# Optimization experiments

Hardware: AMD Instinct MI355X
Metric: run time of the kernel (lower is better)

## Reference

```python
import jax, jax.numpy as jnp
import numpy as np

# --- constants from the module (KANLayer passes degree=3; BSplineActivation defaults) ---
K = 5          # num_control_points
DEG = 3        # degree
G = 3          # grid points (set_grid_points(3) in __init__)
LO, HI = -1.0, 1.0  # grid_range


def basis_table():
    """Precompute the shared [G, K] normalized Gaussian basis table (same for all edges)."""
    knots = np.linspace(LO - DEG * 0.1, HI + DEG * 0.1, K + DEG + 1)
    grid = np.linspace(LO, HI, G)
    bv = np.zeros((G, K), dtype=np.float32)
    for i in range(K):
        center = (knots[i + DEG // 2] + knots[i + DEG // 2 + 1]) / 2.0
        width = (knots[i + DEG + 1] - knots[i]) / 2.0
        bv[:, i] = np.exp(-(((grid - center) / width) ** 2))
    bv = bv / (bv.sum(axis=1, keepdims=True) + 1e-6)
    return jnp.asarray(bv)


def kan_layer(x, cp, bw, sw, imp, bv):
    """Fused KANLayer: x [B,I]; cp [I,J,K]; bw/sw/imp [I,J]; bv [G,K] -> [B,J]."""
    xc = jnp.clip(x, LO, HI)
    gi = (xc - LO) / (HI - LO) * (G - 1)                     # [B,I] in [0, G-1]
    lo = jnp.clip(jnp.floor(gi).astype(jnp.int32), 0, G - 1)
    hi = jnp.clip(jnp.ceil(gi).astype(jnp.int32), 0, G - 1)
    frac = (gi - lo.astype(gi.dtype))[..., None]             # [B,I,1]
    basis = bv[lo] * (1.0 - frac) + bv[hi] * frac            # [B,I,K] gather + lerp
    base = x * jax.nn.sigmoid(x)                             # SiLU base function, [B,I]
    # out[b,j] = sum_i imp[i,j] * (bw[i,j]*base[b,i] + sw[i,j]*basis[b,i,:]@cp[i,j,:])
    out = jnp.einsum('bi,ij->bj', base, imp * bw)
    out = out + jnp.einsum('bik,ijk->bj', basis, imp[:, :, None] * sw[:, :, None] * cp)
    return out


def setup_inputs() -> dict:
    key = jax.random.key(0)
    ks = jax.random.split(key, 9)
    B, D0, D1, D2 = 131072, 64, 128, 64
    return {
        'x': jax.random.normal(ks[0], (B, D0), dtype=jnp.float32),
        'cp0': jax.random.normal(ks[1], (D0, D1, K), dtype=jnp.float32) * 0.1,
        'bw0': jax.random.normal(ks[2], (D0, D1), dtype=jnp.float32),
        'sw0': jax.random.normal(ks[3], (D0, D1), dtype=jnp.float32),
        'imp0': jnp.ones((D0, D1), dtype=jnp.float32),
        'cp1': jax.random.normal(ks[4], (D1, D2, K), dtype=jnp.float32) * 0.1,
        'bw1': jax.random.normal(ks[5], (D1, D2), dtype=jnp.float32),
        'sw1': jax.random.normal(ks[6], (D1, D2), dtype=jnp.float32),
        'imp1': jnp.ones((D1, D2), dtype=jnp.float32),
    }


def reference(x, cp0, bw0, sw0, imp0, cp1, bw1, sw1, imp1):
    bv = basis_table()
    h = kan_layer(x, cp0, bw0, sw0, imp0, bv)
    return kan_layer(h, cp1, bw1, sw1, imp1, bv)
```

## Files before the change

### kernel.cpp

```cpp
#include <hip/hip_runtime.h>
#include <math.h>

typedef __attribute__((ext_vector_type(8))) _Float16 f16x8;
typedef __attribute__((ext_vector_type(2))) _Float16 f16x2;
typedef __attribute__((ext_vector_type(4))) float f32x4;


#define TPB 256
#define BM  128
#define HSTRIDE 272
#define LDS_TOT (128 * HSTRIDE)

__global__ __launch_bounds__(TPB, 2) void kan_mfma_kernel(
    const float* __restrict__ x, const _Float16* __restrict__ W0t,
    const _Float16* __restrict__ W1t, const float* __restrict__ bias0,
    const float* __restrict__ bias1, float* __restrict__ out)
{
    __shared__ char smem[LDS_TOT];
    const int tid  = threadIdx.x;
    const int lane = tid & 63;
    const int wid  = tid >> 6;
    const int gq   = lane >> 4;
    const int lm   = lane & 15;
    const int wavebase = wid * 32;
    const long rowbase = (long)blockIdx.x * BM;

#if __has_builtin(__builtin_amdgcn_cvt_pkrtz)
    auto pk2 = [](float a, float b) -> f16x2 {
        return (f16x2)__builtin_amdgcn_cvt_pkrtz(a, b);
    };
#else
    auto pk2 = [](float a, float b) -> f16x2 {
        return f16x2{(_Float16)a, (_Float16)b};
    };
#endif
#if __has_builtin(__builtin_amdgcn_rcpf)
    auto frcp = [](float a) -> float { return __builtin_amdgcn_rcpf(a); };
#else
    auto frcp = [](float a) -> float { return 1.0f / a; };
#endif

    auto buildFeats4 = [&](const float* v, f16x8* dst) {
        union U { f16x8 v8; f16x2 h2[4]; } u0, u1, u2, u3;
        #pragma unroll
        for (int q = 0; q < 4; ++q) {
            float va = v[2 * q], vb = v[2 * q + 1];
            float ba = va * frcp(1.0f + __expf(-va));
            float bb = vb * frcp(1.0f + __expf(-vb));
            float ga = fminf(fmaxf(va, -1.f), 1.f) + 1.f;
            float gb = fminf(fmaxf(vb, -1.f), 1.f) + 1.f;
            float s1a = (ga >= 1.f) ? 1.f : 0.f;
            float s1b = (gb >= 1.f) ? 1.f : 0.f;
            float sga = (ga >= 1.f) ? ga : 0.f;
            float sgb = (gb >= 1.f) ? gb : 0.f;
            u0.h2[q] = pk2(ba, bb);
            u1.h2[q] = pk2(ga, gb);
            u2.h2[q] = pk2(s1a, s1b);
            u3.h2[q] = pk2(sga, sgb);
        }
        dst[0] = u0.v8; dst[1] = u1.v8; dst[2] = u2.v8; dst[3] = u3.v8;
    };

    float b0v[8], b1v[4];
    #pragma unroll
    for (int nf = 0; nf < 8; ++nf) b0v[nf] = bias0[nf * 16 + lm];
    #pragma unroll
    for (int nf = 0; nf < 4; ++nf) b1v[nf] = bias1[nf * 16 + lm];

    float v0[2][8], v1[2][8];
    #pragma unroll
    for (int mi = 0; mi < 2; ++mi) {
        const float* xp = x + (rowbase + wavebase + mi * 16 + lm) * 64 + gq * 8;
        float4 a0 = *(const float4*)(xp);
        float4 a1 = *(const float4*)(xp + 4);
        float4 a2 = *(const float4*)(xp + 32);
        float4 a3 = *(const float4*)(xp + 36);
        v0[mi][0]=a0.x; v0[mi][1]=a0.y; v0[mi][2]=a0.z; v0[mi][3]=a0.w;
        v0[mi][4]=a1.x; v0[mi][5]=a1.y; v0[mi][6]=a1.z; v0[mi][7]=a1.w;
        v1[mi][0]=a2.x; v1[mi][1]=a2.y; v1[mi][2]=a2.z; v1[mi][3]=a2.w;
        v1[mi][4]=a3.x; v1[mi][5]=a3.y; v1[mi][6]=a3.z; v1[mi][7]=a3.w;
    }

    f32x4 acc[2][8] = {};
    {
        const char* w0 = (const char*)W0t + gq * 2048 + lm * 16;
        f16x8 b0[8], b1[8];
        #pragma unroll
        for (int nf = 0; nf < 8; ++nf) b0[nf] = *(const f16x8*)(w0 + nf * 256);

        f16x8 fr[2][4];
        buildFeats4(v0[0], fr[0]);
        buildFeats4(v0[1], fr[1]);

#define L0_STEP(S, C, CUR, NXT) do {                                          \
        if ((S) < 7) {                                                        \
            _Pragma("unroll")                                                 \
            for (int nf = 0; nf < 8; ++nf)                                    \
                NXT[nf] = *(const f16x8*)(w0 + ((S) + 1) * 8192 + nf * 256);  \
        }                                                                     \
        _Pragma("unroll")                                                     \
        for (int mi = 0; mi < 2; ++mi) {                                      \
            f16x8 a = fr[mi][C];                                              \
            _Pragma("unroll")                                                 \
            for (int nf = 0; nf < 8; ++nf)                                    \
                acc[mi][nf] = __builtin_amdgcn_mfma_f32_16x16x32_f16(         \
                    a, CUR[nf], acc[mi][nf], 0, 0, 0);                        \
        }                                                                     \
    } while (0)

        L0_STEP(0, 0, b0, b1); L0_STEP(1, 1, b1, b0);
        L0_STEP(2, 2, b0, b1); L0_STEP(3, 3, b1, b0);
        buildFeats4(v1[0], fr[0]);
        buildFeats4(v1[1], fr[1]);
        L0_STEP(4, 0, b0, b1); L0_STEP(5, 1, b1, b0);
        L0_STEP(6, 2, b0, b1); L0_STEP(7, 3, b1, b0);
#undef L0_STEP
    }

    #pragma unroll
    for (int mi = 0; mi < 2; ++mi)
        #pragma unroll
        for (int nf = 0; nf < 8; ++nf)
            #pragma unroll
            for (int rg = 0; rg < 4; ++rg)
                *(_Float16*)(smem + (wavebase + mi * 16 + gq * 4 + rg) * HSTRIDE
                             + (nf * 16 + lm) * 2) = (_Float16)(acc[mi][nf][rg] + b0v[nf]);
    __syncthreads();

    f32x4 accO[2][4] = {};
    #pragma unroll
    for (int half = 0; half < 2; ++half) {
        float hv0[2][8], hv1[2][8];
        #pragma unroll
        for (int mi = 0; mi < 2; ++mi) {
            const char* hrow = smem + (wavebase + mi * 16 + lm) * HSTRIDE;
            f16x8 ha = *(const f16x8*)(hrow + (half * 64 + gq * 8) * 2);
            f16x8 hb = *(const f16x8*)(hrow + (half * 64 + 32 + gq * 8) * 2);
            #pragma unroll
            for (int e = 0; e < 8; ++e) { hv0[mi][e] = (float)ha[e]; hv1[mi][e] = (float)hb[e]; }
        }

        const char* w1 = (const char*)W1t + half * 32768 + gq * 1024 + lm * 16;
        f16x8 c0[4], c1[4];
        #pragma unroll
        for (int nf = 0; nf < 4; ++nf) c0[nf] = *(const f16x8*)(w1 + nf * 256);

        f16x8 fr[2][4];
        buildFeats4(hv0[0], fr[0]);
        buildFeats4(hv0[1], fr[1]);

#define L1_STEP(S, C, CUR, NXT) do {                                          \
        if ((S) < 7) {                                                        \
            _Pragma("unroll")                                                 \
            for (int nf = 0; nf < 4; ++nf)                                    \
                NXT[nf] = *(const f16x8*)(w1 + ((S) + 1) * 4096 + nf * 256);  \
        }                                                                     \
        _Pragma("unroll")                                                     \
        for (int mi = 0; mi < 2; ++mi) {                                      \
            f16x8 a = fr[mi][C];                                              \
            _Pragma("unroll")                                                 \
            for (int nf = 0; nf < 4; ++nf)                                    \
                accO[mi][nf] = __builtin_amdgcn_mfma_f32_16x16x32_f16(        \
                    a, CUR[nf], accO[mi][nf], 0, 0, 0);                       \
        }                                                                     \
    } while (0)

        L1_STEP(0, 0, c0, c1); L1_STEP(1, 1, c1, c0);
        L1_STEP(2, 2, c0, c1); L1_STEP(3, 3, c1, c0);
        buildFeats4(hv1[0], fr[0]);
        buildFeats4(hv1[1], fr[1]);
        L1_STEP(4, 0, c0, c1); L1_STEP(5, 1, c1, c0);
        L1_STEP(6, 2, c0, c1); L1_STEP(7, 3, c1, c0);
#undef L1_STEP
    }

    float* og = out + (rowbase + wavebase) * 64;
    #pragma unroll
    for (int mi = 0; mi < 2; ++mi)
        #pragma unroll
        for (int nf = 0; nf < 4; ++nf)
            #pragma unroll
            for (int rg = 0; rg < 4; ++rg)
                og[(mi * 16 + gq * 4 + rg) * 64 + nf * 16 + lm] = accO[mi][nf][rg] + b1v[nf];
}

__global__ __launch_bounds__(256) void kan_combine_w(
    const float* __restrict__ cp0, const float* __restrict__ bw0,
    const float* __restrict__ sw0, const float* __restrict__ imp0,
    const float* __restrict__ cp1, const float* __restrict__ bw1,
    const float* __restrict__ sw1, const float* __restrict__ imp1,
    _Float16* __restrict__ W0t, _Float16* __restrict__ W1t,
    float* __restrict__ bias0, float* __restrict__ bias1)
{
    float bvv[3][5];
    #pragma unroll
    for (int g = 0; g < 3; ++g) {
        float gv = (float)g - 1.0f;
        float e[5]; float s = 0.f;
        #pragma unroll
        for (int i = 0; i < 5; ++i) {
            float cc = -0.8125f + 0.325f * (float)i;
            float d  = (gv - cc) * (1.0f / 0.65f);
            e[i] = __expf(-d * d); s += e[i];
        }
        float inv = 1.0f / (s + 1e-6f);
        #pragma unroll
        for (int i = 0; i < 5; ++i) bvv[g][i] = e[i] * inv;
    }

    auto wval = [&](const float* cp, float bw, float sw, float imp, int q) -> float {
        if (q == 0) return imp * bw;
        float P0 = 0.f, Q0 = 0.f, P1 = 0.f, Q1 = 0.f;
        #pragma unroll
        for (int c = 0; c < 5; ++c) {
            P0 += cp[c] * bvv[0][c];
            Q0 += cp[c] * (bvv[1][c] - bvv[0][c]);
            P1 += cp[c] * (2.f * bvv[1][c] - bvv[2][c]);
            Q1 += cp[c] * (bvv[2][c] - bvv[1][c]);
        }
        float r = (q == 1) ? Q0 : (q == 2) ? (P1 - P0) : (Q1 - Q0);
        return imp * sw * r;
    };
    auto p0val = [&](const float* cp) -> float {
        float P0 = 0.f;
        #pragma unroll
        for (int c = 0; c < 5; ++c) P0 += cp[c] * bvv[0][c];
        return P0;
    };

    const int bx = blockIdx.x;
    const int t  = threadIdx.x;

    if (bx < 256) {
        int f = bx * 256 + t;
        if (f < 32768) {
            int e = f & 7, n = (f >> 3) & 127, g = (f >> 10) & 3, s = f >> 12;
            int ih = s >> 2, q = s & 3;
            int i = ih * 32 + g * 8 + e;
            int edge = i * 128 + n;
            W0t[f] = (_Float16)wval(cp0 + edge * 5, bw0[edge], sw0[edge], imp0[edge], q);
        } else {
            int f2 = f - 32768;
            int e = f2 & 7, n = (f2 >> 3) & 63, g = (f2 >> 9) & 3;
            int tq = f2 >> 11;
            int half = tq >> 3, s = tq & 7;
            int ih = s >> 2, q = s & 3;
            int i2 = half * 64 + ih * 32 + g * 8 + e;
            int edge = i2 * 64 + n;
            W1t[f2] = (_Float16)wval(cp1 + edge * 5, bw1[edge], sw1[edge], imp1[edge], q);
        }
    } else if (bx == 256) {
        __shared__ float part[256];
        int j = t >> 1, h = t & 1;
        float s = 0.f;
        #pragma unroll 4
        for (int i = h * 32; i < h * 32 + 32; ++i) {
            int edge = i * 128 + j;
            s += imp0[edge] * sw0[edge] * p0val(cp0 + edge * 5);
        }
        part[t] = s;
        __syncthreads();
        if (t < 128) bias0[t] = part[2 * t] + part[2 * t + 1];
    } else {
        __shared__ float part[256];
        int j = t >> 2, qtr = t & 3;
        float s = 0.f;
        #pragma unroll 4
        for (int i2 = qtr * 32; i2 < qtr * 32 + 32; ++i2) {
            int edge = i2 * 64 + j;
            s += imp1[edge] * sw1[edge] * p0val(cp1 + edge * 5);
        }
        part[t] = s;
        __syncthreads();
        if (t < 64) bias1[t] = part[4 * t] + part[4 * t + 1] + part[4 * t + 2] + part[4 * t + 3];
    }
}

#define NTHR 256
#define JT 32
#define WS8 8

#define STAGE_L0(JBASE) do {                                                  \
    _Pragma("unroll")                                                         \
    for (int p = 0; p < 8; ++p) {                                             \
        int idx = tid + p * NTHR;                                             \
        int i  = idx >> 5;                                                    \
        int jj = idx & 31;                                                    \
        int e  = i * 128 + (JBASE) + jj;                                      \
        float im = imp0[e];                                                   \
        float wb = bw0[e] * im;                                               \
        float ws = sw0[e] * im;                                               \
        const float* cp = cp0 + e * 5;                                        \
        float* wp = wbuf + idx * WS8;                                         \
        wp[0] = wb;                                                           \
        wp[1] = ws * cp[0]; wp[2] = ws * cp[1]; wp[3] = ws * cp[2];           \
        wp[4] = ws * cp[3]; wp[5] = ws * cp[4];                               \
    }                                                                         \
} while (0)

#define STAGE_L1(IBASE, JBASE) do {                                           \
    _Pragma("unroll")                                                         \
    for (int p = 0; p < 8; ++p) {                                             \
        int idx = tid + p * NTHR;                                             \
        int ii = idx >> 5;                                                    \
        int jj = idx & 31;                                                    \
        int e  = ((IBASE) + ii) * 64 + (JBASE) + jj;                          \
        float im = imp1[e];                                                   \
        float wb = bw1[e] * im;                                               \
        float ws = sw1[e] * im;                                               \
        const float* cp = cp1 + e * 5;                                        \
        float* wp = wbuf + idx * WS8;                                         \
        wp[0] = wb;                                                           \
        wp[1] = ws * cp[0]; wp[2] = ws * cp[1]; wp[3] = ws * cp[2];           \
        wp[4] = ws * cp[3]; wp[5] = ws * cp[4];                               \
    }                                                                         \
} while (0)

#define COMPUTE_TILE(ACC) do {                                                \
    _Pragma("unroll 2")                                                       \
    for (int i = 0; i < 64; ++i) {                                            \
        float v  = vbuf[i][tid];                                              \
        float sg = 1.0f / (1.0f + __expf(-v));                                \
        float base = v * sg;                                                  \
        float xc = fminf(fmaxf(v, -1.0f), 1.0f);                              \
        float gi = xc + 1.0f;                                                 \
        int lo = (int)gi; lo = (lo > 2) ? 2 : lo;                             \
        float fr = gi - (float)lo;                                            \
        int hi = (fr > 0.0f) ? (lo + 1) : lo;                                 \
        float b0 = bvt[lo][0]; b0 += (bvt[hi][0] - b0) * fr;                  \
        float b1 = bvt[lo][1]; b1 += (bvt[hi][1] - b1) * fr;                  \
        float b2 = bvt[lo][2]; b2 += (bvt[hi][2] - b2) * fr;                  \
        float b3 = bvt[lo][3]; b3 += (bvt[hi][3] - b3) * fr;                  \
        float b4 = bvt[lo][4]; b4 += (bvt[hi][4] - b4) * fr;                  \
        const float* wr = wbuf + i * (JT * WS8);                              \
        _Pragma("unroll")                                                     \
        for (int jj = 0; jj < JT; ++jj) {                                     \
            const float* wp = wr + jj * WS8;                                  \
            float a = ACC[jj];                                                \
            a = fmaf(wp[0], base, a);                                         \
            a = fmaf(wp[1], b0, a);                                           \
            a = fmaf(wp[2], b1, a);                                           \
            a = fmaf(wp[3], b2, a);                                           \
            a = fmaf(wp[4], b3, a);                                           \
            a = fmaf(wp[5], b4, a);                                           \
            ACC[jj] = a;                                                      \
        }                                                                     \
    }                                                                         \
} while (0)

__global__ __launch_bounds__(NTHR) void kan_fused_kernel(
    const float* __restrict__ x,
    const float* __restrict__ cp0, const float* __restrict__ bw0,
    const float* __restrict__ sw0, const float* __restrict__ imp0,
    const float* __restrict__ cp1, const float* __restrict__ bw1,
    const float* __restrict__ sw1, const float* __restrict__ imp1,
    float* __restrict__ out)
{
    __shared__ float vbuf[64][NTHR + 1];
    __shared__ float wbuf[64 * JT * WS8];
    __shared__ float bvt[3][8];

    const int tid = threadIdx.x;

    if (tid < 3) {
        float gv = -1.0f + (float)tid;
        float e[5];
        float s = 0.0f;
        #pragma unroll
        for (int i = 0; i < 5; ++i) {
            float c = -0.8125f + 0.325f * (float)i;
            float d = (gv - c) * (1.0f / 0.65f);
            e[i] = expf(-d * d);
            s += e[i];
        }
        float inv = 1.0f / (s + 1e-6f);
        #pragma unroll
        for (int i = 0; i < 5; ++i) bvt[tid][i] = e[i] * inv;
    }

    {
        const float4* xg = (const float4*)(x + (size_t)blockIdx.x * (NTHR * 64));
        #pragma unroll
        for (int it = 0; it < 16; ++it) {
            int e4 = tid + it * NTHR;
            float4 v = xg[e4];
            int r  = e4 >> 4;
            int ib = (e4 & 15) << 2;
            vbuf[ib + 0][r] = v.x;
            vbuf[ib + 1][r] = v.y;
            vbuf[ib + 2][r] = v.z;
            vbuf[ib + 3][r] = v.w;
        }
    }
    __syncthreads();

    float h0[32] = {}, h1[32] = {}, h2[32] = {}, h3[32] = {};
    STAGE_L0(0);   __syncthreads(); COMPUTE_TILE(h0); __syncthreads();
    STAGE_L0(32);  __syncthreads(); COMPUTE_TILE(h1); __syncthreads();
    STAGE_L0(64);  __syncthreads(); COMPUTE_TILE(h2); __syncthreads();
    STAGE_L0(96);  __syncthreads(); COMPUTE_TILE(h3); __syncthreads();

    #pragma unroll
    for (int i = 0; i < 32; ++i) vbuf[i][tid] = h0[i];
    #pragma unroll
    for (int i = 0; i < 32; ++i) vbuf[32 + i][tid] = h1[i];

    float o0[32] = {}, o1[32] = {};
    STAGE_L1(0, 0);   __syncthreads(); COMPUTE_TILE(o0); __syncthreads();
    STAGE_L1(0, 32);  __syncthreads(); COMPUTE_TILE(o1); __syncthreads();

    #pragma unroll
    for (int i = 0; i < 32; ++i) vbuf[i][tid] = h2[i];
    #pragma unroll
    for (int i = 0; i < 32; ++i) vbuf[32 + i][tid] = h3[i];

    STAGE_L1(64, 0);  __syncthreads(); COMPUTE_TILE(o0); __syncthreads();
    STAGE_L1(64, 32); __syncthreads(); COMPUTE_TILE(o1);

    float4* og = (float4*)(out + (size_t)blockIdx.x * (NTHR * 64) + (size_t)tid * 64);
    #pragma unroll
    for (int q = 0; q < 8; ++q)
        og[q] = make_float4(o0[4 * q + 0], o0[4 * q + 1], o0[4 * q + 2], o0[4 * q + 3]);
    #pragma unroll
    for (int q = 0; q < 8; ++q)
        og[8 + q] = make_float4(o1[4 * q + 0], o1[4 * q + 1], o1[4 * q + 2], o1[4 * q + 3]);
}

extern "C" void kernel_launch(void* const* d_in, const int* in_sizes, int n_in,
                              void* d_out, int out_size, void* d_ws, size_t ws_size,
                              hipStream_t stream) {
    const float* x    = (const float*)d_in[0];
    const float* cp0  = (const float*)d_in[1];
    const float* bw0  = (const float*)d_in[2];
    const float* sw0  = (const float*)d_in[3];
    const float* imp0 = (const float*)d_in[4];
    const float* cp1  = (const float*)d_in[5];
    const float* bw1  = (const float*)d_in[6];
    const float* sw1  = (const float*)d_in[7];
    const float* imp1 = (const float*)d_in[8];
    float* out = (float*)d_out;

    const int B = in_sizes[0] / 64;
    const size_t need = 65536 * sizeof(_Float16) + 192 * sizeof(float);

    if (ws_size >= need && (B % BM) == 0) {
        _Float16* W0t = (_Float16*)d_ws;
        _Float16* W1t = W0t + 32768;
        float* bias0 = (float*)(W1t + 32768);
        float* bias1 = bias0 + 128;
        kan_combine_w<<<258, 256, 0, stream>>>(cp0, bw0, sw0, imp0,
                                               cp1, bw1, sw1, imp1,
                                               W0t, W1t, bias0, bias1);
        kan_mfma_kernel<<<B / BM, TPB, 0, stream>>>(x, W0t, W1t, bias0, bias1, out);
    } else {
        kan_fused_kernel<<<B / NTHR, NTHR, 0, stream>>>(
            x, cp0, bw0, sw0, imp0, cp1, bw1, sw1, imp1, out);
    }
}
```

Baseline: 42.11 us.

## Add per-step workgroup barriers in MFMA loops and widen weight-combine blocks

Puts an s_barrier after every MFMA step in both layer loops so the waves of a workgroup stay in lockstep, which may help share cached weight loads between waves. It also relaunches the weight-combine kernel with 1024-thread blocks and 66 blocks instead of 258, and splits the bias reductions across more threads so each one has a shorter serial loop. The barriers add stalls to the hot loop, and the bigger combine blocks may lower occupancy.

```diff
diff --git a/kernel.cpp b/kernel.cpp
--- a/kernel.cpp
+++ b/kernel.cpp
@@ -106,6 +106,7 @@
                 acc[mi][nf] = __builtin_amdgcn_mfma_f32_16x16x32_f16(         \
                     a, CUR[nf], acc[mi][nf], 0, 0, 0);                        \
         }                                                                     \
+        __builtin_amdgcn_s_barrier();    \
     } while (0)
 
         L0_STEP(0, 0, b0, b1); L0_STEP(1, 1, b1, b0);
@@ -163,6 +164,7 @@
                 accO[mi][nf] = __builtin_amdgcn_mfma_f32_16x16x32_f16(        \
                     a, CUR[nf], accO[mi][nf], 0, 0, 0);                       \
         }                                                                     \
+        __builtin_amdgcn_s_barrier();                                         \
     } while (0)
 
         L1_STEP(0, 0, c0, c1); L1_STEP(1, 1, c1, c0);
@@ -184,7 +186,7 @@
                 og[(mi * 16 + gq * 4 + rg) * 64 + nf * 16 + lm] = accO[mi][nf][rg] + b1v[nf];
 }
 
-__global__ __launch_bounds__(256) void kan_combine_w(
+__global__ __launch_bounds__(1024) void kan_combine_w(
     const float* __restrict__ cp0, const float* __restrict__ bw0,
     const float* __restrict__ sw0, const float* __restrict__ imp0,
     const float* __restrict__ cp1, const float* __restrict__ bw1,
@@ -231,8 +233,8 @@
     const int bx = blockIdx.x;
     const int t  = threadIdx.x;
 
-    if (bx < 256) {
-        int f = bx * 256 + t;
+    if (bx < 64) {
+        int f = bx * 1024 + t;
         if (f < 32768) {
             int e = f & 7, n = (f >> 3) & 127, g = (f >> 10) & 3, s = f >> 12;
             int ih = s >> 2, q = s & 3;
@@ -249,30 +251,42 @@
             int edge = i2 * 64 + n;
             W1t[f2] = (_Float16)wval(cp1 + edge * 5, bw1[edge], sw1[edge], imp1[edge], q);
         }
-    } else if (bx == 256) {
-        __shared__ float part[256];
-        int j = t >> 1, h = t & 1;
+    } else if (bx == 64) {
+        __shared__ float part[1024];
+        int j = t >> 3, split = t & 7;
         float s = 0.f;
-        #pragma unroll 4
-        for (int i = h * 32; i < h * 32 + 32; ++i) {
+        #pragma unroll
+        for (int k = 0; k < 8; ++k) {
+            int i = split * 8 + k;
             int edge = i * 128 + j;
             s += imp0[edge] * sw0[edge] * p0val(cp0 + edge * 5);
         }
         part[t] = s;
         __syncthreads();
-        if (t < 128) bias0[t] = part[2 * t] + part[2 * t + 1];
+        if (t < 128) {
+            float acc = 0.f;
+            #pragma unroll
+            for (int k = 0; k < 8; ++k) acc += part[t * 8 + k];
+            bias0[t] = acc;
+        }
     } else {
-        __shared__ float part[256];
-        int j = t >> 2, qtr = t & 3;
+        __shared__ float part[1024];
+        int j = t >> 4, split = t & 15;
         float s = 0.f;
-        #pragma unroll 4
-        for (int i2 = qtr * 32; i2 < qtr * 32 + 32; ++i2) {
+        #pragma unroll
+        for (int k = 0; k < 8; ++k) {
+            int i2 = split * 8 + k;
             int edge = i2 * 64 + j;
             s += imp1[edge] * sw1[edge] * p0val(cp1 + edge * 5);
         }
         part[t] = s;
         __syncthreads();
-        if (t < 64) bias1[t] = part[4 * t] + part[4 * t + 1] + part[4 * t + 2] + part[4 * t + 3];
+        if (t < 64) {
+            float acc = 0.f;
+            #pragma unroll
+            for (int k = 0; k < 16; ++k) acc += part[t * 16 + k];
+            bias1[t] = acc;
+        }
     }
 }
 
@@ -448,7 +462,7 @@
         _Float16* W1t = W0t + 32768;
         float* bias0 = (float*)(W1t + 32768);
         float* bias1 = bias0 + 128;
-        kan_combine_w<<<258, 256, 0, stream>>>(cp0, bw0, sw0, imp0,
+        kan_combine_w<<<66, 1024, 0, stream>>>(cp0, bw0, sw0, imp0,
                                                cp1, bw1, sw1, imp1,
                                                W0t, W1t, bias0, bias1);
         kan_mfma_kernel<<<B / BM, TPB, 0, stream>>>(x, W0t, W1t, bias0, bias1, out);
```

Result: slower. 49.65 us (+17.9%).

## Stage MFMA weight tiles through double-buffered LDS and parallelize bias reduction

Applied to the files above, without the earlier changes.

Previously each wave loaded its B-operand weight fragments straight from global memory, so all four waves re-read the same weights. The new code has the whole block cooperatively copy each weight chunk into a double-buffered LDS region, with prefetch into registers and a __syncthreads per step. This cuts redundant global/L2 traffic but adds 8+16 block barriers and grows LDS from about 35KB to about 51KB. The bias-reduction blocks in the combine kernel are also spread across 16+16 blocks instead of 2 to shorten that serial tail.

```diff
diff --git a/kernel.cpp b/kernel.cpp
--- a/kernel.cpp
+++ b/kernel.cpp
@@ -9,7 +9,8 @@
 #define TPB 256
 #define BM  128
 #define HSTRIDE 272
-#define LDS_TOT (128 * HSTRIDE)
+#define W_OFF   34816
+#define LDS_TOT (34816 + 16384)
 
 __global__ __launch_bounds__(TPB, 2) void kan_mfma_kernel(
     const float* __restrict__ x, const _Float16* __restrict__ W0t,
@@ -83,95 +84,120 @@
 
     f32x4 acc[2][8] = {};
     {
-        const char* w0 = (const char*)W0t + gq * 2048 + lm * 16;
-        f16x8 b0[8], b1[8];
-        #pragma unroll
-        for (int nf = 0; nf < 8; ++nf) b0[nf] = *(const f16x8*)(w0 + nf * 256);
-
+        const char* w0 = (const char*)W0t;
+        const int lb0 = (gq * 128 + lm) * 16;
+
+        {
+            float4 pa = *(const float4*)(w0 + tid * 32);
+            float4 pb = *(const float4*)(w0 + tid * 32 + 16);
+            *(float4*)(smem + W_OFF + tid * 32)      = pa;
+            *(float4*)(smem + W_OFF + tid * 32 + 16) = pb;
+        }
         f16x8 fr[2][4];
         buildFeats4(v0[0], fr[0]);
         buildFeats4(v0[1], fr[1]);
-
-#define L0_STEP(S, C, CUR, NXT) do {                                          \
+        __syncthreads();
+
+        float4 wr0, wr1;
+#define L0_STEP(S, C) do {                                                    \
         if ((S) < 7) {                                                        \
-            _Pragma("unroll")                                                 \
-            for (int nf = 0; nf < 8; ++nf)                                    \
-                NXT[nf] = *(const f16x8*)(w0 + ((S) + 1) * 8192 + nf * 256);  \
+            wr0 = *(const float4*)(w0 + ((S) + 1) * 8192 + tid * 32);         \
+            wr1 = *(const float4*)(w0 + ((S) + 1) * 8192 + tid * 32 + 16);    \
         }                                                                     \
+        const char* wb = smem + W_OFF + ((S) & 1) * 8192;                     \
+        f16x8 bt[8];                                                          \
+        _Pragma("unroll")                                                     \
+        for (int nf = 0; nf < 8; ++nf)                                        \
+            bt[nf] = *(const f16x8*)(wb + lb0 + nf * 256);                    \
         _Pragma("unroll")                                                     \
         for (int mi = 0; mi < 2; ++mi) {                                      \
             f16x8 a = fr[mi][C];                                              \
             _Pragma("unroll")                                                 \
             for (int nf = 0; nf < 8; ++nf)                                    \
                 acc[mi][nf] = __builtin_amdgcn_mfma_f32_16x16x32_f16(         \
-                    a, CUR[nf], acc[mi][nf], 0, 0, 0);                        \
+                    a, bt[nf], acc[mi][nf], 0, 0, 0);                         \
         }                                                                     \
+        if ((S) < 7) {                                                        \
+            char* nb = smem + W_OFF + (((S) + 1) & 1) * 8192;                 \
+            *(float4*)(nb + tid * 32)      = wr0;                             \
+            *(float4*)(nb + tid * 32 + 16) = wr1;                             \
+        }                                                                     \
+        __syncthreads();                                                      \
     } while (0)
 
-        L0_STEP(0, 0, b0, b1); L0_STEP(1, 1, b1, b0);
-        L0_STEP(2, 2, b0, b1); L0_STEP(3, 3, b1, b0);
+        L0_STEP(0, 0); L0_STEP(1, 1); L0_STEP(2, 2); L0_STEP(3, 3);
         buildFeats4(v1[0], fr[0]);
         buildFeats4(v1[1], fr[1]);
-        L0_STEP(4, 0, b0, b1); L0_STEP(5, 1, b1, b0);
-        L0_STEP(6, 2, b0, b1); L0_STEP(7, 3, b1, b0);
+        L0_STEP(4, 0); L0_STEP(5, 1); L0_STEP(6, 2); L0_STEP(7, 3);
 #undef L0_STEP
     }
 
-    #pragma unroll
-    for (int mi = 0; mi < 2; ++mi)
-        #pragma unroll
-        for (int nf = 0; nf < 8; ++nf)
+    {
+        const char* w1 = (const char*)W1t;
+        float4 p0 = *(const float4*)(w1 + tid * 16);
+        #pragma unroll
+        for (int mi = 0; mi < 2; ++mi)
             #pragma unroll
-            for (int rg = 0; rg < 4; ++rg)
-                *(_Float16*)(smem + (wavebase + mi * 16 + gq * 4 + rg) * HSTRIDE
-                             + (nf * 16 + lm) * 2) = (_Float16)(acc[mi][nf][rg] + b0v[nf]);
-    __syncthreads();
+            for (int nf = 0; nf < 8; ++nf)
+                #pragma unroll
+                for (int rg = 0; rg < 4; ++rg)
+                    *(_Float16*)(smem + (wavebase + mi * 16 + gq * 4 + rg) * HSTRIDE
+                                 + (nf * 16 + lm) * 2) = (_Float16)(acc[mi][nf][rg] + b0v[nf]);
+        __syncthreads();
+        *(float4*)(smem + W_OFF + tid * 16) = p0;
+        __syncthreads();
+    }
 
     f32x4 accO[2][4] = {};
-    #pragma unroll
-    for (int half = 0; half < 2; ++half) {
-        float hv0[2][8], hv1[2][8];
-        #pragma unroll
-        for (int mi = 0; mi < 2; ++mi) {
-            const char* hrow = smem + (wavebase + mi * 16 + lm) * HSTRIDE;
-            f16x8 ha = *(const f16x8*)(hrow + (half * 64 + gq * 8) * 2);
-            f16x8 hb = *(const f16x8*)(hrow + (half * 64 + 32 + gq * 8) * 2);
-            #pragma unroll
-            for (int e = 0; e < 8; ++e) { hv0[mi][e] = (float)ha[e]; hv1[mi][e] = (float)hb[e]; }
-        }
-
-        const char* w1 = (const char*)W1t + half * 32768 + gq * 1024 + lm * 16;
-        f16x8 c0[4], c1[4];
-        #pragma unroll
-        for (int nf = 0; nf < 4; ++nf) c0[nf] = *(const f16x8*)(w1 + nf * 256);
-
+    {
+        const char* w1 = (const char*)W1t;
+        const int lb1 = (gq * 64 + lm) * 16;
         f16x8 fr[2][4];
-        buildFeats4(hv0[0], fr[0]);
-        buildFeats4(hv0[1], fr[1]);
-
-#define L1_STEP(S, C, CUR, NXT) do {                                          \
-        if ((S) < 7) {                                                        \
-            _Pragma("unroll")                                                 \
-            for (int nf = 0; nf < 4; ++nf)                                    \
-                NXT[nf] = *(const f16x8*)(w1 + ((S) + 1) * 4096 + nf * 256);  \
-        }                                                                     \
+        float4 wr0;
+
+#define L1_STEP(CI, C) do {                                                   \
+        if ((CI) < 15)                                                        \
+            wr0 = *(const float4*)(w1 + ((CI) + 1) * 4096 + tid * 16);        \
+        const char* wb = smem + W_OFF + ((CI) & 1) * 8192;                    \
+        f16x8 bt[4];                                                          \
+        _Pragma("unroll")                                                     \
+        for (int nf = 0; nf < 4; ++nf)                                        \
+            bt[nf] = *(const f16x8*)(wb + lb1 + nf * 256);                    \
         _Pragma("unroll")                                                     \
         for (int mi = 0; mi < 2; ++mi) {                                      \
             f16x8 a = fr[mi][C];                                              \
             _Pragma("unroll")                                                 \
             for (int nf = 0; nf < 4; ++nf)                                    \
                 accO[mi][nf] = __builtin_amdgcn_mfma_f32_16x16x32_f16(        \
-                    a, CUR[nf], accO[mi][nf], 0, 0, 0);                       \
+                    a, bt[nf], accO[mi][nf], 0, 0, 0);                        \
+        }                                                                     \
+        if ((CI) < 15)                                                        \
+            *(float4*)(smem + W_OFF + (((CI) + 1) & 1) * 8192 + tid * 16) = wr0; \
+        __syncthreads();                                                      \
+    } while (0)
+
+#define L1_FEATS(HALF, IH) do {                                               \
+        _Pragma("unroll")                                                     \
+        for (int mi = 0; mi < 2; ++mi) {                                      \
+            const char* hrow = smem + (wavebase + mi * 16 + lm) * HSTRIDE;    \
+            f16x8 hv = *(const f16x8*)(hrow + ((HALF) * 64 + (IH) * 32 + gq * 8) * 2); \
+            float v[8];                                                       \
+            _Pragma("unroll")                                                 \
+            for (int e = 0; e < 8; ++e) v[e] = (float)hv[e];                  \
+            buildFeats4(v, fr[mi]);                                           \
         }                                                                     \
     } while (0)
 
-        L1_STEP(0, 0, c0, c1); L1_STEP(1, 1, c1, c0);
-        L1_STEP(2, 2, c0, c1); L1_STEP(3, 3, c1, c0);
-        buildFeats4(hv1[0], fr[0]);
-        buildFeats4(hv1[1], fr[1]);
-        L1_STEP(4, 0, c0, c1); L1_STEP(5, 1, c1, c0);
-        L1_STEP(6, 2, c0, c1); L1_STEP(7, 3, c1, c0);
+        L1_FEATS(0, 0);
+        L1_STEP(0, 0);  L1_STEP(1, 1);  L1_STEP(2, 2);  L1_STEP(3, 3);
+        L1_FEATS(0, 1);
+        L1_STEP(4, 0);  L1_STEP(5, 1);  L1_STEP(6, 2);  L1_STEP(7, 3);
+        L1_FEATS(1, 0);
+        L1_STEP(8, 0);  L1_STEP(9, 1);  L1_STEP(10, 2); L1_STEP(11, 3);
+        L1_FEATS(1, 1);
+        L1_STEP(12, 0); L1_STEP(13, 1); L1_STEP(14, 2); L1_STEP(15, 3);
 #undef L1_STEP
+#undef L1_FEATS
     }
 
     float* og = out + (rowbase + wavebase) * 64;
@@ -249,30 +275,46 @@
             int edge = i2 * 64 + n;
             W1t[f2] = (_Float16)wval(cp1 + edge * 5, bw1[edge], sw1[edge], imp1[edge], q);
         }
-    } else if (bx == 256) {
+    } else if (bx < 272) {
         __shared__ float part[256];
-        int j = t >> 1, h = t & 1;
+        int bb = bx - 256;
+        int jj = t >> 5, split = t & 31;
+        int j = bb * 8 + jj;
         float s = 0.f;
-        #pragma unroll 4
-        for (int i = h * 32; i < h * 32 + 32; ++i) {
+        #pragma unroll
+        for (int k = 0; k < 2; ++k) {
+            int i = split * 2 + k;
             int edge = i * 128 + j;
             s += imp0[edge] * sw0[edge] * p0val(cp0 + edge * 5);
         }
         part[t] = s;
         __syncthreads();
-        if (t < 128) bias0[t] = part[2 * t] + part[2 * t + 1];
+        if (t < 8) {
+            float acc = 0.f;
+            #pragma unroll
+            for (int k = 0; k < 32; ++k) acc += part[t * 32 + k];
+            bias0[bb * 8 + t] = acc;
+        }
     } else {
         __shared__ float part[256];
-        int j = t >> 2, qtr = t & 3;
+        int bb = bx - 272;
+        int jj = t >> 6, split = t & 63;
+        int j = bb * 4 + jj;
         float s = 0.f;
-        #pragma unroll 4
-        for (int i2 = qtr * 32; i2 < qtr * 32 + 32; ++i2) {
+        #pragma unroll
+        for (int k = 0; k < 2; ++k) {
+            int i2 = split * 2 + k;
             int edge = i2 * 64 + j;
             s += imp1[edge] * sw1[edge] * p0val(cp1 + edge * 5);
         }
         part[t] = s;
         __syncthreads();
-        if (t < 64) bias1[t] = part[4 * t] + part[4 * t + 1] + part[4 * t + 2] + part[4 * t + 3];
+        if (t < 4) {
+            float acc = 0.f;
+            #pragma unroll
+            for (int k = 0; k < 64; ++k) acc += part[t * 64 + k];
+            bias1[bb * 4 + t] = acc;
+        }
     }
 }
 
@@ -448,7 +490,7 @@
         _Float16* W1t = W0t + 32768;
         float* bias0 = (float*)(W1t + 32768);
         float* bias1 = bias0 + 128;
-        kan_combine_w<<<258, 256, 0, stream>>>(cp0, bw0, sw0, imp0,
+        kan_combine_w<<<288, 256, 0, stream>>>(cp0, bw0, sw0, imp0,
                                                cp1, bw1, sw1, imp1,
                                                W0t, W1t, bias0, bias1);
         kan_mfma_kernel<<<B / BM, TPB, 0, stream>>>(x, W0t, W1t, bias0, bias1, out);
```

After: 37.58 us. 10.8% less time.
